# Performance work log

Hardware: AMD Instinct MI355X
Metric: run time of the kernel (lower is better)

The kernel has to match this reference:

```python
import jax, jax.numpy as jnp
import numpy as np

K = 7          # involution kernel size
GC = 16        # group_channels (hardcoded in module)
BN_EPS = 1e-5
LN_EPS = 1e-6


def _forward(x, conv1_w, conv1_b, bn_gamma, bn_beta, bn_mean, bn_var,
             conv2_w, conv2_b, ln_w, ln_b, w1, b1, w2, b2):
    b, c, h, w = x.shape
    groups = c // GC
    # --- involution: dynamic kernel generation (1x1 conv -> BN(eval) -> ReLU -> 1x1 conv) ---
    t = jnp.einsum('bchw,oc->bohw', x, conv1_w) + conv1_b[None, :, None, None]
    t = (t - bn_mean[None, :, None, None]) * (bn_gamma / jnp.sqrt(bn_var + BN_EPS))[None, :, None, None] \
        + bn_beta[None, :, None, None]
    t = jax.nn.relu(t)
    wgt = jnp.einsum('bchw,oc->bohw', t, conv2_w) + conv2_b[None, :, None, None]
    wgt = wgt.reshape(b, groups, K * K, h, w)                  # (b,g,k2,h,w)
    # --- unfold: gather kxk neighborhoods (channel-major, then kh, kw — matches torch Unfold) ---
    p = (K - 1) // 2
    xp = jnp.pad(x, ((0, 0), (0, 0), (p, p), (p, p)))
    patches = jnp.stack([xp[:, :, i:i + h, j:j + w]
                         for i in range(K) for j in range(K)], axis=2)   # (b,c,k2,h,w)
    patches = patches.reshape(b, groups, GC, K * K, h, w)
    # weighted sum over kernel positions
    out = jnp.einsum('bgkhw,bgckhw->bgchw', wgt, patches).reshape(b, c, h, w)
    # --- LN + MLP residual (channels_last) ---
    y = out.transpose(0, 2, 3, 1)                               # (b,h,w,c)
    mu = y.mean(-1, keepdims=True)
    var = ((y - mu) ** 2).mean(-1, keepdims=True)
    y = (y - mu) / jnp.sqrt(var + LN_EPS) * ln_w + ln_b
    y = jax.nn.gelu(y @ w1.T + b1, approximate=False)           # torch GELU = exact erf
    y = y @ w2.T + b2                                           # dropout_rate=0 -> identity
    return y.transpose(0, 3, 1, 2) + x


def setup_inputs() -> dict:
    key = jax.random.key(0)
    ks = jax.random.split(key, 6)
    dim = 128
    groups = dim // GC
    red = dim // 4
    b, h, w = 8, 56, 56
    return {
        'x': jax.random.normal(ks[0], (b, dim, h, w), jnp.float32),
        'conv1_w': jax.random.normal(ks[1], (red, dim), jnp.float32) * (1.0 / np.sqrt(dim)),
        'conv1_b': jnp.zeros((red,), jnp.float32),
        'bn_gamma': jnp.ones((red,), jnp.float32),
        'bn_beta': jnp.zeros((red,), jnp.float32),
        'bn_mean': jnp.zeros((red,), jnp.float32),
        'bn_var': jnp.ones((red,), jnp.float32),
        'conv2_w': jax.random.normal(ks[2], (K * K * groups, red), jnp.float32) * (1.0 / np.sqrt(red)),
        'conv2_b': jnp.zeros((K * K * groups,), jnp.float32),
        'ln_w': jnp.ones((dim,), jnp.float32),
        'ln_b': jnp.zeros((dim,), jnp.float32),
        'w1': jax.random.normal(ks[3], (4 * dim, dim), jnp.float32) * (1.0 / np.sqrt(dim)),
        'b1': jnp.zeros((4 * dim,), jnp.float32),
        'w2': jax.random.normal(ks[4], (dim, 4 * dim), jnp.float32) * (1.0 / np.sqrt(4 * dim)),
        'b2': jnp.zeros((dim,), jnp.float32),
    }


def reference(x, conv1_w, conv1_b, bn_gamma, bn_beta, bn_mean, bn_var,
              conv2_w, conv2_b, ln_w, ln_b, w1, b1, w2, b2):
    return _forward(x, conv1_w, conv1_b, bn_gamma, bn_beta, bn_mean, bn_var,
                    conv2_w, conv2_b, ln_w, ln_b, w1, b1, w2, b2)
```

## Files before the change

### kernel.cpp

```cpp
#include <hip/hip_runtime.h>
#include <hip/hip_bf16.h>
#include <math.h>

#define HW    3136
#define WIMG  56
#define NPIX  25088
#define CIN   128
#define RED   32
#define NGROUP 8
#define GCH   16
#define KKK   49
#define TP    32

typedef __attribute__((ext_vector_type(8))) short short8;
typedef __attribute__((ext_vector_type(4))) float f32x4;
typedef unsigned short ushort_t;

static __device__ __forceinline__ unsigned int f2b(float f) {
    union { __hip_bfloat16 b; unsigned short u; } cv;
    cv.b = __float2bfloat16(f);
    return (unsigned int)cv.u;
}

static __device__ __forceinline__ float gelu_t(float h) {
    float z = h * fmaf(0.0356774081f, h * h, 0.7978845608f);
    float e = __expf(-2.f * z);
    return __fdividef(h, 1.f + e);
}

__global__ __launch_bounds__(256) void k_prep(const float* __restrict__ conv1_w,
    const float* __restrict__ conv1_b, const float* __restrict__ bn_g,
    const float* __restrict__ bn_b, const float* __restrict__ bn_m,
    const float* __restrict__ bn_v, const float* __restrict__ conv2_w,
    const float* __restrict__ ln_w, const float* __restrict__ w1,
    const float* __restrict__ w2,
    ushort_t* __restrict__ c1b, ushort_t* __restrict__ c2b,
    ushort_t* __restrict__ lw1b, ushort_t* __restrict__ w2b,
    float* __restrict__ sc1, float* __restrict__ sh1)
{
    int id = blockIdx.x * 256 + threadIdx.x;
    w2b[id] = (ushort_t)f2b(w2[id]);
    int c = id & 127;
    lw1b[id] = (ushort_t)f2b(w1[id] * ln_w[c]);
    if (id < 4096)  c1b[id] = (ushort_t)f2b(conv1_w[id]);
    if (id < 12800) c2b[id] = (id < 12544) ? (ushort_t)f2b(conv2_w[id]) : (ushort_t)0;
    if (id < 32) {
        float sc = bn_g[id] * rsqrtf(bn_v[id] + 1e-5f);
        sc1[id] = sc;
        sh1[id] = (conv1_b[id] - bn_m[id]) * sc + bn_b[id];
    }
}

__global__ void k_prep2(const float* __restrict__ w1, const float* __restrict__ ln_w,
    const float* __restrict__ ln_b, const float* __restrict__ b1,
    float* __restrict__ s1, float* __restrict__ t1)
{
    int n = threadIdx.x;
    const float* wr = w1 + (size_t)n * 128;
    float s = 0.f, t = 0.f;
    #pragma unroll 8
    for (int c = 0; c < 128; ++c) { float w = wr[c]; s += ln_w[c] * w; t += ln_b[c] * w; }
    s1[n] = s; t1[n] = t + b1[n];
}

__global__ __launch_bounds__(256) void k_mega(const float* __restrict__ x,
    const short* __restrict__ c1b, const short* __restrict__ c2b,
    const float* __restrict__ sc1, const float* __restrict__ sh1,
    const float* __restrict__ c2bias,
    const ushort_t* __restrict__ lw1b, const ushort_t* __restrict__ w2b,
    const float* __restrict__ s1, const float* __restrict__ t1,
    const float* __restrict__ b2, float* __restrict__ outp)
{
    __shared__ __align__(16) char smem[44608];
    short* swg  = (short*)smem;
    short* sh   = (short*)smem;
    short* sx   = (short*)(smem + 27200);
    short* st   = (short*)(smem + 35904);
    float* sred  = (float*)(smem + 35904);
    float* sred2 = sred + 1056;
    float* smu   = sred2 + 1056;
    float* srs   = smu + 32;

    int tid  = threadIdx.x;
    int P0   = blockIdx.x * TP;
    int b    = P0 / HW;
    int p0i  = P0 - b * HW;
    int lane = tid & 63, wv = tid >> 6;
    int ln15 = lane & 15, quad = lane >> 4;

    const float* xb = x + (size_t)b * CIN * HW + p0i;
    #pragma unroll
    for (int it = 0; it < 16; ++it) {
        int idx = it * 256 + tid;
        int c = idx >> 5, pp = idx & 31;
        sx[pp * 136 + c] = (short)f2b(xb[(size_t)c * HW + pp]);
    }
    __syncthreads();

    {
        int mt = wv & 1, nt = wv >> 1;
        f32x4 a1 = (f32x4)0.f;
        #pragma unroll
        for (int kc = 0; kc < 128; kc += 32) {
            short8 af = *(const short8*)&sx[(mt * 16 + ln15) * 136 + kc + quad * 8];
            short8 bf = *(const short8*)&c1b[(size_t)(nt * 16 + ln15) * 128 + kc + quad * 8];
            a1 = __builtin_amdgcn_mfma_f32_16x16x32_bf16(af, bf, a1, 0, 0, 0);
        }
        int o = nt * 16 + ln15;
        float sc = sc1[o], shv = sh1[o];
        #pragma unroll
        for (int r = 0; r < 4; ++r) {
            float tv = fmaxf(a1[r] * sc + shv, 0.f);
            st[(mt * 16 + quad * 4 + r) * 40 + o] = (short)f2b(tv);
        }
    }
    __syncthreads();

    {
        short8 af2[2];
        #pragma unroll
        for (int mt = 0; mt < 2; ++mt)
            af2[mt] = *(const short8*)&st[(mt * 16 + ln15) * 40 + quad * 8];
        f32x4 zc = (f32x4)0.f;
        for (int nt = wv; nt < 25; nt += 4) {
            int gk = nt * 16 + ln15;
            short8 bf2 = *(const short8*)&c2b[(size_t)gk * 32 + quad * 8];
            float bj = (gk < 392) ? c2bias[gk] : 0.f;
            #pragma unroll
            for (int mt = 0; mt < 2; ++mt) {
                f32x4 a2 = __builtin_amdgcn_mfma_f32_16x16x32_bf16(af2[mt], bf2, zc, 0, 0, 0);
                uint2 pk;
                pk.x = f2b(a2[0] + bj) | (f2b(a2[1] + bj) << 16);
                pk.y = f2b(a2[2] + bj) | (f2b(a2[3] + bj) << 16);
                *(uint2*)&swg[gk * 34 + mt * 16 + quad * 4] = pk;
            }
        }
    }
    __syncthreads();

    {
        int q   = tid & 7;
        int gy  = tid >> 3;
        int g   = gy >> 2;
        int sub = gy & 3;
        int pl0 = q * 4;
        int p   = p0i + pl0;
        int prow = p / WIMG;
        int pcol = p - prow * WIMG;
        const float* xc = x + ((size_t)b * CIN + g * GCH + sub * 4) * HW;
        float acc[4][4];
        #pragma unroll
        for (int i = 0; i < 4; ++i)
            #pragma unroll
            for (int c = 0; c < 4; ++c) acc[i][c] = 0.f;
        bool c_lo = (pcol >= 4);
        bool c_hi = (pcol <= 48);
        #pragma unroll
        for (int dy = -3; dy <= 3; ++dy) {
            int grow = prow + dy;
            if (grow < 0 || grow >= WIMG) continue;
            float wkf[7][4];
            #pragma unroll
            for (int dx = 0; dx < 7; ++dx) {
                int gk = g * KKK + (dy + 3) * 7 + dx;
                uint2 wld = *(const uint2*)&swg[gk * 34 + pl0];
                wkf[dx][0] = __uint_as_float(wld.x << 16);
                wkf[dx][1] = __uint_as_float(wld.x & 0xffff0000u);
                wkf[dx][2] = __uint_as_float(wld.y << 16);
                wkf[dx][3] = __uint_as_float(wld.y & 0xffff0000u);
            }
            const float* xrow = xc + grow * WIMG + pcol;
            #pragma unroll
            for (int c = 0; c < 4; ++c) {
                const float* xr = xrow + (size_t)c * HW;
                float4 v0 = c_lo ? *(const float4*)(xr - 4) : make_float4(0.f,0.f,0.f,0.f);
                float4 v1 = *(const float4*)(xr);
                float4 v2 = c_hi ? *(const float4*)(xr + 4) : make_float4(0.f,0.f,0.f,0.f);
                float vv[12] = {v0.x,v0.y,v0.z,v0.w, v1.x,v1.y,v1.z,v1.w, v2.x,v2.y,v2.z,v2.w};
                #pragma unroll
                for (int dx = 0; dx < 7; ++dx)
                    #pragma unroll
                    for (int i = 0; i < 4; ++i)
                        acc[i][c] += wkf[dx][i] * vv[i + dx + 1];
            }
        }
        #pragma unroll
        for (int i = 0; i < 4; ++i) {
            float s = 0.f, s2 = 0.f;
            #pragma unroll
            for (int c = 0; c < 4; ++c) { s += acc[i][c]; s2 += acc[i][c] * acc[i][c]; }
            uint2 pk;
            pk.x = f2b(acc[i][0]) | (f2b(acc[i][1]) << 16);
            pk.y = f2b(acc[i][2]) | (f2b(acc[i][3]) << 16);
            *(uint2*)&sx[(pl0 + i) * 136 + g * GCH + sub * 4] = pk;
            sred [(pl0 + i) * 33 + gy] = s;
            sred2[(pl0 + i) * 33 + gy] = s2;
        }
    }
    __syncthreads();

    if (tid < TP) {
        float s = 0.f, s2 = 0.f;
        #pragma unroll
        for (int gy = 0; gy < 32; ++gy) { s += sred[tid * 33 + gy]; s2 += sred2[tid * 33 + gy]; }
        float m = s * (1.f / 128.f);
        float v = s2 * (1.f / 128.f) - m * m;
        smu[tid] = m;
        srs[tid] = rsqrtf(v + 1e-6f);
    }
    __syncthreads();

    float mu_r[2], rs_r[2];
    #pragma unroll
    for (int tn = 0; tn < 2; ++tn) {
        int px = tn * 16 + ln15;
        mu_r[tn] = smu[px];
        rs_r[tn] = srs[px];
    }

    f32x4 acc2[2][2];
    #pragma unroll
    for (int i = 0; i < 2; ++i)
        #pragma unroll
        for (int j = 0; j < 2; ++j) acc2[i][j] = (f32x4)0.f;

    for (int j = 0; j < 4; ++j) {
        f32x4 acc1[2][2];
        #pragma unroll
        for (int tm = 0; tm < 2; ++tm)
            #pragma unroll
            for (int tn = 0; tn < 2; ++tn) acc1[tm][tn] = (f32x4)0.f;
        #pragma unroll
        for (int kc = 0; kc < 128; kc += 32) {
            short8 af[2], bf[2];
            #pragma unroll
            for (int tm = 0; tm < 2; ++tm)
                af[tm] = *(const short8*)&lw1b[(size_t)(j * 128 + wv * 32 + tm * 16 + ln15) * 128 + kc + quad * 8];
            #pragma unroll
            for (int tn = 0; tn < 2; ++tn)
                bf[tn] = *(const short8*)&sx[(tn * 16 + ln15) * 136 + kc + quad * 8];
            #pragma unroll
            for (int tm = 0; tm < 2; ++tm)
                #pragma unroll
                for (int tn = 0; tn < 2; ++tn)
                    acc1[tm][tn] = __builtin_amdgcn_mfma_f32_16x16x32_bf16(af[tm], bf[tn], acc1[tm][tn], 0, 0, 0);
        }
        #pragma unroll
        for (int tm = 0; tm < 2; ++tm) {
            int nl = wv * 32 + tm * 16 + quad * 4;
            int n  = j * 128 + nl;
            float4 s14 = *(const float4*)&s1[n];
            float4 t14 = *(const float4*)&t1[n];
            #pragma unroll
            for (int tn = 0; tn < 2; ++tn) {
                int px = tn * 16 + ln15;
                float g0 = gelu_t(rs_r[tn] * (acc1[tm][tn][0] - mu_r[tn] * s14.x) + t14.x);
                float g1 = gelu_t(rs_r[tn] * (acc1[tm][tn][1] - mu_r[tn] * s14.y) + t14.y);
                float g2 = gelu_t(rs_r[tn] * (acc1[tm][tn][2] - mu_r[tn] * s14.z) + t14.z);
                float g3 = gelu_t(rs_r[tn] * (acc1[tm][tn][3] - mu_r[tn] * s14.w) + t14.w);
                uint2 pk;
                pk.x = f2b(g0) | (f2b(g1) << 16);
                pk.y = f2b(g2) | (f2b(g3) << 16);
                *(uint2*)&sh[px * 136 + nl] = pk;
            }
        }
        __syncthreads();
        #pragma unroll
        for (int kc = 0; kc < 128; kc += 32) {
            short8 af[2], bf[2];
            #pragma unroll
            for (int tm = 0; tm < 2; ++tm)
                af[tm] = *(const short8*)&sh[(tm * 16 + ln15) * 136 + kc + quad * 8];
            #pragma unroll
            for (int tn = 0; tn < 2; ++tn)
                bf[tn] = *(const short8*)&w2b[(size_t)(wv * 32 + tn * 16 + ln15) * 512 + j * 128 + kc + quad * 8];
            #pragma unroll
            for (int tm = 0; tm < 2; ++tm)
                #pragma unroll
                for (int tn = 0; tn < 2; ++tn)
                    acc2[tm][tn] = __builtin_amdgcn_mfma_f32_16x16x32_bf16(af[tm], bf[tn], acc2[tm][tn], 0, 0, 0);
        }
        __syncthreads();
    }

    #pragma unroll
    for (int tm = 0; tm < 2; ++tm) {
        int p = p0i + tm * 16 + quad * 4;
        #pragma unroll
        for (int tn = 0; tn < 2; ++tn) {
            int c = wv * 32 + tn * 16 + ln15;
            size_t base = ((size_t)b * CIN + c) * HW + p;
            float bj = b2[c];
            float4 rv = *(const float4*)&x[base];
            float4 ov = make_float4(acc2[tm][tn][0] + bj + rv.x,
                                    acc2[tm][tn][1] + bj + rv.y,
                                    acc2[tm][tn][2] + bj + rv.z,
                                    acc2[tm][tn][3] + bj + rv.w);
            *(float4*)&outp[base] = ov;
        }
    }
}

extern "C" void kernel_launch(void* const* d_in, const int* in_sizes, int n_in,
                              void* d_out, int out_size, void* d_ws, size_t ws_size,
                              hipStream_t stream) {
    const float* x       = (const float*)d_in[0];
    const float* conv1_w = (const float*)d_in[1];
    const float* conv1_b = (const float*)d_in[2];
    const float* bn_g    = (const float*)d_in[3];
    const float* bn_b    = (const float*)d_in[4];
    const float* bn_m    = (const float*)d_in[5];
    const float* bn_v    = (const float*)d_in[6];
    const float* conv2_w = (const float*)d_in[7];
    const float* conv2_b = (const float*)d_in[8];
    const float* ln_w    = (const float*)d_in[9];
    const float* ln_b    = (const float*)d_in[10];
    const float* w1      = (const float*)d_in[11];
    const float* b1      = (const float*)d_in[12];
    const float* w2      = (const float*)d_in[13];
    const float* b2      = (const float*)d_in[14];
    float* out = (float*)d_out;

    float* F = (float*)d_ws;
    float* sc1  = F;
    float* sh1  = F + 32;
    float* s1   = F + 64;
    float* t1   = F + 576;
    ushort_t* S    = (ushort_t*)(F + 1088);
    ushort_t* c1b  = S;
    ushort_t* c2b  = c1b + 4096;
    ushort_t* lw1b = c2b + 12800;
    ushort_t* w2b  = lw1b + 65536;

    k_prep <<<256, 256, 0, stream>>>(conv1_w, conv1_b, bn_g, bn_b, bn_m, bn_v,
                                     conv2_w, ln_w, w1, w2, c1b, c2b, lw1b, w2b, sc1, sh1);
    k_prep2<<<1, 512, 0, stream>>>(w1, ln_w, ln_b, b1, s1, t1);
    k_mega <<<784, 256, 0, stream>>>(x, (const short*)c1b, (const short*)c2b,
                                     sc1, sh1, conv2_b, lw1b, w2b, s1, t1, b2, out);
}
```

Baseline: 173.8 us.

## Prefetch MLP weight fragments, remove LN stats barrier, swizzle block order

```diff
diff --git a/kernel.cpp b/kernel.cpp
--- a/kernel.cpp
+++ b/kernel.cpp
@@ -71,18 +71,18 @@
     const float* __restrict__ s1, const float* __restrict__ t1,
     const float* __restrict__ b2, float* __restrict__ outp)
 {
-    __shared__ __align__(16) char smem[44608];
+    __shared__ __align__(16) char smem[45120];
     short* swg  = (short*)smem;
     short* sh   = (short*)smem;
     short* sx   = (short*)(smem + 27200);
     short* st   = (short*)(smem + 35904);
     float* sred  = (float*)(smem + 35904);
-    float* sred2 = sred + 1056;
-    float* smu   = sred2 + 1056;
-    float* srs   = smu + 32;
+    float* sred2 = sred + 1152;
 
     int tid  = threadIdx.x;
-    int P0   = blockIdx.x * TP;
+    int bid  = blockIdx.x;
+    int sblk = (bid & 7) * 98 + (bid >> 3);
+    int P0   = sblk * TP;
     int b    = P0 / HW;
     int p0i  = P0 - b * HW;
     int lane = tid & 63, wv = tid >> 6;
@@ -193,20 +193,9 @@
             pk.x = f2b(acc[i][0]) | (f2b(acc[i][1]) << 16);
             pk.y = f2b(acc[i][2]) | (f2b(acc[i][3]) << 16);
             *(uint2*)&sx[(pl0 + i) * 136 + g * GCH + sub * 4] = pk;
-            sred [(pl0 + i) * 33 + gy] = s;
-            sred2[(pl0 + i) * 33 + gy] = s2;
-        }
-    }
-    __syncthreads();
-
-    if (tid < TP) {
-        float s = 0.f, s2 = 0.f;
-        #pragma unroll
-        for (int gy = 0; gy < 32; ++gy) { s += sred[tid * 33 + gy]; s2 += sred2[tid * 33 + gy]; }
-        float m = s * (1.f / 128.f);
-        float v = s2 * (1.f / 128.f) - m * m;
-        smu[tid] = m;
-        srs[tid] = rsqrtf(v + 1e-6f);
+            sred [(pl0 + i) * 36 + gy] = s;
+            sred2[(pl0 + i) * 36 + gy] = s2;
+        }
     }
     __syncthreads();
 
@@ -214,8 +203,17 @@
     #pragma unroll
     for (int tn = 0; tn < 2; ++tn) {
         int px = tn * 16 + ln15;
-        mu_r[tn] = smu[px];
-        rs_r[tn] = srs[px];
+        float s = 0.f, s2 = 0.f;
+        #pragma unroll
+        for (int k4 = 0; k4 < 8; ++k4) {
+            float4 a = *(const float4*)&sred [px * 36 + k4 * 4];
+            float4 c = *(const float4*)&sred2[px * 36 + k4 * 4];
+            s  += a.x + a.y + a.z + a.w;
+            s2 += c.x + c.y + c.z + c.w;
+        }
+        float m = s * (1.f / 128.f);
+        mu_r[tn] = m;
+        rs_r[tn] = rsqrtf(s2 * (1.f / 128.f) - m * m + 1e-6f);
     }
 
     f32x4 acc2[2][2];
@@ -225,25 +223,32 @@
         for (int j = 0; j < 2; ++j) acc2[i][j] = (f32x4)0.f;
 
     for (int j = 0; j < 4; ++j) {
+        short8 a1f[4][2], b2f[4][2];
+        #pragma unroll
+        for (int k4 = 0; k4 < 4; ++k4) {
+            #pragma unroll
+            for (int tm = 0; tm < 2; ++tm)
+                a1f[k4][tm] = *(const short8*)&lw1b[(size_t)(j * 128 + wv * 32 + tm * 16 + ln15) * 128 + k4 * 32 + quad * 8];
+            #pragma unroll
+            for (int tn = 0; tn < 2; ++tn)
+                b2f[k4][tn] = *(const short8*)&w2b[(size_t)(wv * 32 + tn * 16 + ln15) * 512 + j * 128 + k4 * 32 + quad * 8];
+        }
         f32x4 acc1[2][2];
         #pragma unroll
         for (int tm = 0; tm < 2; ++tm)
             #pragma unroll
             for (int tn = 0; tn < 2; ++tn) acc1[tm][tn] = (f32x4)0.f;
         #pragma unroll
-        for (int kc = 0; kc < 128; kc += 32) {
-            short8 af[2], bf[2];
-            #pragma unroll
-            for (int tm = 0; tm < 2; ++tm)
-                af[tm] = *(const short8*)&lw1b[(size_t)(j * 128 + wv * 32 + tm * 16 + ln15) * 128 + kc + quad * 8];
+        for (int k4 = 0; k4 < 4; ++k4) {
+            short8 bf[2];
             #pragma unroll
             for (int tn = 0; tn < 2; ++tn)
-                bf[tn] = *(const short8*)&sx[(tn * 16 + ln15) * 136 + kc + quad * 8];
+                bf[tn] = *(const short8*)&sx[(tn * 16 + ln15) * 136 + k4 * 32 + quad * 8];
             #pragma unroll
             for (int tm = 0; tm < 2; ++tm)
                 #pragma unroll
                 for (int tn = 0; tn < 2; ++tn)
-                    acc1[tm][tn] = __builtin_amdgcn_mfma_f32_16x16x32_bf16(af[tm], bf[tn], acc1[tm][tn], 0, 0, 0);
+                    acc1[tm][tn] = __builtin_amdgcn_mfma_f32_16x16x32_bf16(a1f[k4][tm], bf[tn], acc1[tm][tn], 0, 0, 0);
         }
         #pragma unroll
         for (int tm = 0; tm < 2; ++tm) {
@@ -266,19 +271,16 @@
         }
         __syncthreads();
         #pragma unroll
-        for (int kc = 0; kc < 128; kc += 32) {
-            short8 af[2], bf[2];
+        for (int k4 = 0; k4 < 4; ++k4) {
+            short8 af[2];
             #pragma unroll
             for (int tm = 0; tm < 2; ++tm)
-                af[tm] = *(const short8*)&sh[(tm * 16 + ln15) * 136 + kc + quad * 8];
-            #pragma unroll
-            for (int tn = 0; tn < 2; ++tn)
-                bf[tn] = *(const short8*)&w2b[(size_t)(wv * 32 + tn * 16 + ln15) * 512 + j * 128 + kc + quad * 8];
+                af[tm] = *(const short8*)&sh[(tm * 16 + ln15) * 136 + k4 * 32 + quad * 8];
             #pragma unroll
             for (int tm = 0; tm < 2; ++tm)
                 #pragma unroll
                 for (int tn = 0; tn < 2; ++tn)
-                    acc2[tm][tn] = __builtin_amdgcn_mfma_f32_16x16x32_bf16(af[tm], bf[tn], acc2[tm][tn], 0, 0, 0);
+                    acc2[tm][tn] = __builtin_amdgcn_mfma_f32_16x16x32_bf16(af[tm], b2f[k4][tn], acc2[tm][tn], 0, 0, 0);
         }
         __syncthreads();
     }
```

Result: faster. 167.9 us (-3.4%).
